# Optimization experiments

Hardware: AMD Instinct MI355X
Metric: run time of the kernel (lower is better)

The kernel has to match this reference:

```python
import jax, jax.numpy as jnp
import numpy as np

N = 4194304  # batch of 2-D points
N_NODE = 16
N_INT = 5


def setup_inputs() -> dict:
    key = jax.random.key(0)
    k1, k2, k3, k4 = jax.random.split(key, 4)
    # Kaiming-ish small init so ReLU chain doesn't blow up
    x = jax.random.normal(k1, (N, 2), dtype=jnp.float32)
    w_in = jax.random.normal(k2, (N_NODE, 2), dtype=jnp.float32) * (1.0 / np.sqrt(2.0))
    w_mid = jax.random.normal(k3, (N_INT, N_NODE, N_NODE), dtype=jnp.float32) * (1.0 / np.sqrt(N_NODE))
    w_out = jax.random.normal(k4, (2, N_NODE), dtype=jnp.float32) * (1.0 / np.sqrt(N_NODE))
    return {"x": x, "w_in": w_in, "w_mid": w_mid, "w_out": w_out}


def reference(x, w_in, w_mid, w_out):
    # Linear(2,16,bias=False) + ReLU
    h = jax.nn.relu(x @ w_in.T)  # [N, 16]
    def step(h, w):
        return jax.nn.relu(h @ w.T), None
    h, _ = jax.lax.scan(step, h, w_mid)
    # final Linear(16,2,bias=False), no activation
    return h @ w_out.T  # [N, 2]
```

## Files before the change

### kernel.cpp

```cpp
#include <hip/hip_runtime.h>


typedef _Float16 h4v __attribute__((ext_vector_type(4)));
typedef float f4 __attribute__((ext_vector_type(4)));
typedef float f2 __attribute__((ext_vector_type(2)));
typedef unsigned int u32;
typedef u32 u2v __attribute__((ext_vector_type(2)));

static __device__ __forceinline__ f4 mfma16(h4v a, h4v b, f4 c) {
    return __builtin_amdgcn_mfma_f32_16x16x16f16(a, b, c, 0, 0, 0);
}

static __device__ __forceinline__ u32 cvtpk(float a, float b) {
    return __builtin_bit_cast(u32, __builtin_amdgcn_cvt_pkrtz(a, b));
}

static __device__ __forceinline__ h4v pack2(u32 lo, u32 hi) {
    u2v p = {lo, hi};
    return __builtin_bit_cast(h4v, p);
}

static __device__ __forceinline__ h4v wfrag(const float* row, int g) {
    const f4* r4 = (const f4*)row;
    f4 q = r4[g];
    return pack2(cvtpk(q.x, q.y), cvtpk(q.z, q.w));
}

static __device__ __forceinline__ h4v cvt_relu4(f4 a) {
    h4v hb = pack2(cvtpk(a[0], a[1]), cvtpk(a[2], a[3]));
    const h4v z = {};
    return __builtin_elementwise_max(hb, z);
}

__global__ __launch_bounds__(256, 5) void denoiser_mfma16(
    const f2* __restrict__ x,
    const float* __restrict__ w_in,
    const float* __restrict__ w_mid,
    const float* __restrict__ w_out,
    f2* __restrict__ out,
    int n)
{
    const int lane = threadIdx.x & 63;
    const int nn   = lane & 15;
    const int g    = lane >> 4;
    const int wave = threadIdx.x >> 6;

    const h4v hz = {};

    u32 wxy = cvtpk(w_in[2 * nn], w_in[2 * nn + 1]);
    h4v wi0 = g == 0 ? pack2(wxy, 0u) : hz;
    h4v wi1 = g == 1 ? pack2(wxy, 0u) : hz;
    h4v wi2 = g == 2 ? pack2(wxy, 0u) : hz;
    h4v wi3 = g == 3 ? pack2(wxy, 0u) : hz;

    h4v wm0 = wfrag(w_mid + 0 * 256 + nn * 16, g);
    h4v wm1 = wfrag(w_mid + 1 * 256 + nn * 16, g);
    h4v wm2 = wfrag(w_mid + 2 * 256 + nn * 16, g);
    h4v wm3 = wfrag(w_mid + 3 * 256 + nn * 16, g);
    h4v wm4 = wfrag(w_mid + 4 * 256 + nn * 16, g);

    h4v wo = nn < 2 ? wfrag(w_out + nn * 16, g) : hz;

    f4 z4 = {};
    asm("" : "+v"(z4));

    const int nchunks = (n + 255) >> 8;
    const int stride  = gridDim.x;
    const int nm1     = n - 1;

    auto loadx = [&](int c) -> f2 {
        int pi = c * 256 + wave * 64 + lane;
        return x[pi < n ? pi : nm1];
    };

    int c = blockIdx.x;
    f2 xy = loadx(c);

    for (; c < nchunks; c += stride) {
        const int cn = c + stride;
        f2 xyn = loadx(cn < nchunks ? cn : c);

        const int base = c * 256 + wave * 64;

        h4v bin = pack2(cvtpk(xy.x, xy.y), 0u);
        f4 a0 = mfma16(wi0, bin, z4);
        f4 a1 = mfma16(wi1, bin, z4);
        f4 a2 = mfma16(wi2, bin, z4);
        f4 a3 = mfma16(wi3, bin, z4);
        h4v b0 = cvt_relu4(a0);
        h4v b1 = cvt_relu4(a1);
        h4v b2 = cvt_relu4(a2);
        h4v b3 = cvt_relu4(a3);

        a0 = mfma16(wm0, b0, z4);  a1 = mfma16(wm0, b1, z4);
        a2 = mfma16(wm0, b2, z4);  a3 = mfma16(wm0, b3, z4);
        b0 = cvt_relu4(a0);  b1 = cvt_relu4(a1);
        b2 = cvt_relu4(a2);  b3 = cvt_relu4(a3);

        a0 = mfma16(wm1, b0, z4);  a1 = mfma16(wm1, b1, z4);
        a2 = mfma16(wm1, b2, z4);  a3 = mfma16(wm1, b3, z4);
        b0 = cvt_relu4(a0);  b1 = cvt_relu4(a1);
        b2 = cvt_relu4(a2);  b3 = cvt_relu4(a3);

        a0 = mfma16(wm2, b0, z4);  a1 = mfma16(wm2, b1, z4);
        a2 = mfma16(wm2, b2, z4);  a3 = mfma16(wm2, b3, z4);
        b0 = cvt_relu4(a0);  b1 = cvt_relu4(a1);
        b2 = cvt_relu4(a2);  b3 = cvt_relu4(a3);

        a0 = mfma16(wm3, b0, z4);  a1 = mfma16(wm3, b1, z4);
        a2 = mfma16(wm3, b2, z4);  a3 = mfma16(wm3, b3, z4);
        b0 = cvt_relu4(a0);  b1 = cvt_relu4(a1);
        b2 = cvt_relu4(a2);  b3 = cvt_relu4(a3);

        a0 = mfma16(wm4, b0, z4);  a1 = mfma16(wm4, b1, z4);
        a2 = mfma16(wm4, b2, z4);  a3 = mfma16(wm4, b3, z4);
        b0 = cvt_relu4(a0);  b1 = cvt_relu4(a1);
        b2 = cvt_relu4(a2);  b3 = cvt_relu4(a3);

        a0 = mfma16(wo, b0, z4);
        a1 = mfma16(wo, b1, z4);
        a2 = mfma16(wo, b2, z4);
        a3 = mfma16(wo, b3, z4);

        if (lane < 16) {
            int p0 = base + nn;
            if (base + 64 <= n) {
                out[p0]      = (f2){a0[0], a0[1]};
                out[p0 + 16] = (f2){a1[0], a1[1]};
                out[p0 + 32] = (f2){a2[0], a2[1]};
                out[p0 + 48] = (f2){a3[0], a3[1]};
            } else {
                if (p0 < n)      out[p0]      = (f2){a0[0], a0[1]};
                if (p0 + 16 < n) out[p0 + 16] = (f2){a1[0], a1[1]};
                if (p0 + 32 < n) out[p0 + 32] = (f2){a2[0], a2[1]};
                if (p0 + 48 < n) out[p0 + 48] = (f2){a3[0], a3[1]};
            }
        }

        xy = xyn;
    }
}

extern "C" void kernel_launch(void* const* d_in, const int* in_sizes, int n_in,
                              void* d_out, int out_size, void* d_ws, size_t ws_size,
                              hipStream_t stream) {
    const float* x     = (const float*)d_in[0];
    const float* w_in  = (const float*)d_in[1];
    const float* w_mid = (const float*)d_in[2];
    const float* w_out = (const float*)d_in[3];

    int n = in_sizes[0] / 2;
    int nchunks = (n + 255) / 256;
    int blocks = nchunks < 2048 ? nchunks : 2048;

    denoiser_mfma16<<<blocks, 256, 0, stream>>>(
        (const f2*)x, w_in, w_mid, w_out, (f2*)d_out, n);
}
```

Measured before the change: 27.66 us.

## Process two 64-point tiles per wave and pack output into all lanes

Each wave now handles 128 points per iteration as two independent MFMA chains, giving more instruction-level parallelism between dependent MFMA and convert steps. The final layer uses per-lane-group selected output weights so every one of the 64 lanes writes one coalesced output, instead of only 16 lanes doing strided stores. The cost is more registers, so the occupancy hint is lowered from 5 to 4 waves per SIMD.

```diff
diff --git a/kernel.cpp b/kernel.cpp
--- a/kernel.cpp
+++ b/kernel.cpp
@@ -32,7 +32,7 @@
     return __builtin_elementwise_max(hb, z);
 }
 
-__global__ __launch_bounds__(256, 5) void denoiser_mfma16(
+__global__ __launch_bounds__(256, 4) void denoiser_mfma16(
     const f2* __restrict__ x,
     const float* __restrict__ w_in,
     const float* __restrict__ w_mid,
@@ -48,10 +48,11 @@
     const h4v hz = {};
 
     u32 wxy = cvtpk(w_in[2 * nn], w_in[2 * nn + 1]);
-    h4v wi0 = g == 0 ? pack2(wxy, 0u) : hz;
-    h4v wi1 = g == 1 ? pack2(wxy, 0u) : hz;
-    h4v wi2 = g == 2 ? pack2(wxy, 0u) : hz;
-    h4v wi3 = g == 3 ? pack2(wxy, 0u) : hz;
+    h4v wiv = pack2(wxy, 0u);
+    h4v wi0 = g == 0 ? wiv : hz;
+    h4v wi1 = g == 1 ? wiv : hz;
+    h4v wi2 = g == 2 ? wiv : hz;
+    h4v wi3 = g == 3 ? wiv : hz;
 
     h4v wm0 = wfrag(w_mid + 0 * 256 + nn * 16, g);
     h4v wm1 = wfrag(w_mid + 1 * 256 + nn * 16, g);
@@ -59,85 +60,97 @@
     h4v wm3 = wfrag(w_mid + 3 * 256 + nn * 16, g);
     h4v wm4 = wfrag(w_mid + 4 * 256 + nn * 16, g);
 
-    h4v wo = nn < 2 ? wfrag(w_out + nn * 16, g) : hz;
+    h4v wofull = (nn & 3) < 2 ? wfrag(w_out + (nn & 3) * 16, g) : hz;
+    int tsel = nn >> 2;
+    h4v wo0 = tsel == 0 ? wofull : hz;
+    h4v wo1 = tsel == 1 ? wofull : hz;
+    h4v wo2 = tsel == 2 ? wofull : hz;
+    h4v wo3 = tsel == 3 ? wofull : hz;
 
     f4 z4 = {};
     asm("" : "+v"(z4));
 
-    const int nchunks = (n + 255) >> 8;
+    const int nchunks = (n + 511) >> 9;
     const int stride  = gridDim.x;
     const int nm1     = n - 1;
 
-    auto loadx = [&](int c) -> f2 {
-        int pi = c * 256 + wave * 64 + lane;
+    auto loadx = [&](int c, int half) -> f2 {
+        int pi = c * 512 + wave * 128 + half * 64 + lane;
         return x[pi < n ? pi : nm1];
     };
 
+    auto selstore = [&](f4 a0, f4 a1, f4 a2, f4 a3) -> f2 {
+        float s0 = g < 2 ? (g == 1 ? a1[0] : a0[0]) : (g == 3 ? a3[0] : a2[0]);
+        float s1 = g < 2 ? (g == 1 ? a1[1] : a0[1]) : (g == 3 ? a3[1] : a2[1]);
+        return (f2){s0, s1};
+    };
+
     int c = blockIdx.x;
-    f2 xy = loadx(c);
+    f2 xyA = loadx(c, 0);
+    f2 xyB = loadx(c, 1);
 
     for (; c < nchunks; c += stride) {
         const int cn = c + stride;
-        f2 xyn = loadx(cn < nchunks ? cn : c);
+        const int cp = cn < nchunks ? cn : c;
+        f2 xyA2 = loadx(cp, 0);
+        f2 xyB2 = loadx(cp, 1);
 
-        const int base = c * 256 + wave * 64;
+        const int base = c * 512 + wave * 128;
+        const bool full = (base + 128 <= n);
 
-        h4v bin = pack2(cvtpk(xy.x, xy.y), 0u);
-        f4 a0 = mfma16(wi0, bin, z4);
-        f4 a1 = mfma16(wi1, bin, z4);
-        f4 a2 = mfma16(wi2, bin, z4);
-        f4 a3 = mfma16(wi3, bin, z4);
-        h4v b0 = cvt_relu4(a0);
-        h4v b1 = cvt_relu4(a1);
-        h4v b2 = cvt_relu4(a2);
-        h4v b3 = cvt_relu4(a3);
+        h4v binA = pack2(cvtpk(xyA.x, xyA.y), 0u);
+        h4v binB = pack2(cvtpk(xyB.x, xyB.y), 0u);
+        f4 a0 = mfma16(wi0, binA, z4);
+        f4 a1 = mfma16(wi1, binA, z4);
+        f4 a2 = mfma16(wi2, binA, z4);
+        f4 a3 = mfma16(wi3, binA, z4);
+        f4 a4 = mfma16(wi0, binB, z4);
+        f4 a5 = mfma16(wi1, binB, z4);
+        f4 a6 = mfma16(wi2, binB, z4);
+        f4 a7 = mfma16(wi3, binB, z4);
+        h4v b0 = cvt_relu4(a0), b1 = cvt_relu4(a1);
+        h4v b2 = cvt_relu4(a2), b3 = cvt_relu4(a3);
+        h4v b4 = cvt_relu4(a4), b5 = cvt_relu4(a5);
+        h4v b6 = cvt_relu4(a6), b7 = cvt_relu4(a7);
 
-        a0 = mfma16(wm0, b0, z4);  a1 = mfma16(wm0, b1, z4);
-        a2 = mfma16(wm0, b2, z4);  a3 = mfma16(wm0, b3, z4);
-        b0 = cvt_relu4(a0);  b1 = cvt_relu4(a1);
-        b2 = cvt_relu4(a2);  b3 = cvt_relu4(a3);
+        #define MIDLAYER(W)                                        \
+            a0 = mfma16(W, b0, z4);  a1 = mfma16(W, b1, z4);       \
+            a2 = mfma16(W, b2, z4);  a3 = mfma16(W, b3, z4);       \
+            a4 = mfma16(W, b4, z4);  a5 = mfma16(W, b5, z4);       \
+            a6 = mfma16(W, b6, z4);  a7 = mfma16(W, b7, z4);       \
+            b0 = cvt_relu4(a0);  b1 = cvt_relu4(a1);               \
+            b2 = cvt_relu4(a2);  b3 = cvt_relu4(a3);               \
+            b4 = cvt_relu4(a4);  b5 = cvt_relu4(a5);               \
+            b6 = cvt_relu4(a6);  b7 = cvt_relu4(a7);
+        MIDLAYER(wm0)
+        MIDLAYER(wm1)
+        MIDLAYER(wm2)
+        MIDLAYER(wm3)
+        MIDLAYER(wm4)
+        #undef MIDLAYER
 
-        a0 = mfma16(wm1, b0, z4);  a1 = mfma16(wm1, b1, z4);
-        a2 = mfma16(wm1, b2, z4);  a3 = mfma16(wm1, b3, z4);
-        b0 = cvt_relu4(a0);  b1 = cvt_relu4(a1);
-        b2 = cvt_relu4(a2);  b3 = cvt_relu4(a3);
+        a0 = mfma16(wo0, b0, z4);
+        a1 = mfma16(wo1, b1, z4);
+        a2 = mfma16(wo2, b2, z4);
+        a3 = mfma16(wo3, b3, z4);
+        a4 = mfma16(wo0, b4, z4);
+        a5 = mfma16(wo1, b5, z4);
+        a6 = mfma16(wo2, b6, z4);
+        a7 = mfma16(wo3, b7, z4);
 
-        a0 = mfma16(wm2, b0, z4);  a1 = mfma16(wm2, b1, z4);
-        a2 = mfma16(wm2, b2, z4);  a3 = mfma16(wm2, b3, z4);
-        b0 = cvt_relu4(a0);  b1 = cvt_relu4(a1);
-        b2 = cvt_relu4(a2);  b3 = cvt_relu4(a3);
+        f2 oA = selstore(a0, a1, a2, a3);
+        f2 oB = selstore(a4, a5, a6, a7);
 
-        a0 = mfma16(wm3, b0, z4);  a1 = mfma16(wm3, b1, z4);
-        a2 = mfma16(wm3, b2, z4);  a3 = mfma16(wm3, b3, z4);
-        b0 = cvt_relu4(a0);  b1 = cvt_relu4(a1);
-        b2 = cvt_relu4(a2);  b3 = cvt_relu4(a3);
-
-        a0 = mfma16(wm4, b0, z4);  a1 = mfma16(wm4, b1, z4);
-        a2 = mfma16(wm4, b2, z4);  a3 = mfma16(wm4, b3, z4);
-        b0 = cvt_relu4(a0);  b1 = cvt_relu4(a1);
-        b2 = cvt_relu4(a2);  b3 = cvt_relu4(a3);
-
-        a0 = mfma16(wo, b0, z4);
-        a1 = mfma16(wo, b1, z4);
-        a2 = mfma16(wo, b2, z4);
-        a3 = mfma16(wo, b3, z4);
-
-        if (lane < 16) {
-            int p0 = base + nn;
-            if (base + 64 <= n) {
-                out[p0]      = (f2){a0[0], a0[1]};
-                out[p0 + 16] = (f2){a1[0], a1[1]};
-                out[p0 + 32] = (f2){a2[0], a2[1]};
-                out[p0 + 48] = (f2){a3[0], a3[1]};
-            } else {
-                if (p0 < n)      out[p0]      = (f2){a0[0], a0[1]};
-                if (p0 + 16 < n) out[p0 + 16] = (f2){a1[0], a1[1]};
-                if (p0 + 32 < n) out[p0 + 32] = (f2){a2[0], a2[1]};
-                if (p0 + 48 < n) out[p0 + 48] = (f2){a3[0], a3[1]};
-            }
+        if (full) {
+            out[base + lane]      = oA;
+            out[base + 64 + lane] = oB;
+        } else {
+            if (base + lane < n)      out[base + lane]      = oA;
+            if (base + 64 + lane < n) out[base + 64 + lane] = oB;
         }
 
-        xy = xyn;
+        xyA = xyA2;
+        xyB = xyB2;
     }
 }
 
@@ -150,7 +163,7 @@
     const float* w_out = (const float*)d_in[3];
 
     int n = in_sizes[0] / 2;
-    int nchunks = (n + 255) / 256;
+    int nchunks = (n + 511) / 512;
     int blocks = nchunks < 2048 ? nchunks : 2048;
 
     denoiser_mfma16<<<blocks, 256, 0, stream>>>(
```

Result: no change. 27.75 us (+0.3%).
